# Kernel tuning notes

Hardware: AMD Instinct MI355X
Metric: run time of the kernel (lower is better)

## Reference

```python
import math
import jax, jax.numpy as jnp
import numpy as np

# ---------------- static structure (mirrors CG_woFilter_cuda + MyBatchNormWeightMM) ----------------
LMAX = 4
TAUS = [16, 16, 16, 16, 16]          # t_F: input channels per degree l
T_O  = [16, 16, 16, 16, 16]          # output channels per degree l after weight matmul
BN_EPS = 1e-5

# all (l, l1, l2) triples with l2 <= l1 <= lmax and |l1-l2| <= l <= min(l1+l2, lmax), sorted by (l,l1,l2)
TRIPLES = sorted([(l, l1, l2)
                  for l1 in range(LMAX + 1)
                  for l2 in range(l1 + 1)
                  for l in range(l1 - l2, min(l1 + l2, LMAX) + 1)])

T_FF = [0] * (LMAX + 1)              # t_FF[l] = sum over triples of taus[l1]*taus[l2]
for (l, l1, l2) in TRIPLES:
    T_FF[l] += TAUS[l1] * TAUS[l2]

def _cg_coef(j1, m1, j2, m2, j, m):
    """Clebsch-Gordan coefficient <j1 m1 j2 m2 | j m> (Condon-Shortley)."""
    if m1 + m2 != m:
        return 0.0
    f = math.factorial
    if j < abs(j1 - j2) or j > j1 + j2:
        return 0.0
    pref = math.sqrt((2 * j + 1) * f(j + j1 - j2) * f(j - j1 + j2) * f(j1 + j2 - j) / f(j1 + j2 + j + 1))
    pref *= math.sqrt(f(j + m) * f(j - m) * f(j1 - m1) * f(j1 + m1) * f(j2 - m2) * f(j2 + m2))
    s = 0.0
    for k in range(0, j1 + j2 - j + 1):
        if (j1 - m1 - k) < 0 or (j2 + m2 - k) < 0 or (j - j2 + m1 + k) < 0 or (j - j1 - m2 + k) < 0:
            continue
        s += ((-1.0) ** k) / (f(k) * f(j1 + j2 - j - k) * f(j1 - m1 - k)
                              * f(j2 + m2 - k) * f(j - j2 + m1 + k) * f(j - j1 - m2 + k))
    return pref * s

def _cg_matrix(l, l1, l2):
    C = np.zeros((2 * l + 1, 2 * l1 + 1, 2 * l2 + 1), dtype=np.float32)
    for m in range(-l, l + 1):
        for m1 in range(-l1, l1 + 1):
            m2 = m - m1
            if -l2 <= m2 <= l2:
                C[m + l, m1 + l1, m2 + l2] = _cg_coef(l1, m1, l2, m2, l, m)
    return C

CG_MATS = {t: jnp.asarray(_cg_matrix(*t)) for t in TRIPLES}

M_IN = sum(TAUS[l] * (2 * l + 1) for l in range(LMAX + 1))      # 400
W_LEN = sum(T_FF[l] * T_O[l] for l in range(LMAX + 1))          # 172032


def setup_inputs() -> dict:
    key = jax.random.key(0)
    k1, k2 = jax.random.split(key)
    B = 256
    Fs = jax.random.normal(k1, (B, M_IN, 2), dtype=jnp.float32)
    W = jax.random.normal(k2, (W_LEN, 2), dtype=jnp.float32) * 0.05
    return {"Fs": Fs, "W": W}


def reference(Fs, W):
    B = Fs.shape[0]
    # split input into per-degree blocks: F_l [B, tau, 2l+1, 2]
    Fl, off = [], 0
    for l in range(LMAX + 1):
        n = TAUS[l] * (2 * l + 1)
        Fl.append(Fs[:, off:off + n, :].reshape(B, TAUS[l], 2 * l + 1, 2))
        off += n
    # sparse CG tensor product: per-triple complex outer product contracted with CG coefs
    frags = [[] for _ in range(LMAX + 1)]
    for (l, l1, l2) in TRIPLES:
        C = CG_MATS[(l, l1, l2)]                     # [2l+1, 2l1+1, 2l2+1]
        a, b = Fl[l1], Fl[l2]
        ar, ai = a[..., 0], a[..., 1]
        br, bi = b[..., 0], b[..., 1]
        rr = jnp.einsum('bip,bjq,mpq->bijm', ar, br, C)
        ii = jnp.einsum('bip,bjq,mpq->bijm', ai, bi, C)
        ri = jnp.einsum('bip,bjq,mpq->bijm', ar, bi, C)
        ir = jnp.einsum('bip,bjq,mpq->bijm', ai, br, C)
        fr = (rr - ii).reshape(B, -1, 2 * l + 1)     # channels flattened as c1*tau2 + c2 (t_offsets order)
        fi = (ri + ir).reshape(B, -1, 2 * l + 1)
        frags[l].append(jnp.stack([fr, fi], axis=-1))
    # per-degree fragment batchnorm + complex weight matmul (FN_WMM)
    outs, woff = [], 0
    for l in range(LMAX + 1):
        FF = jnp.concatenate(frags[l], axis=1)       # [B, t_FF, 2l+1, 2]
        var = jnp.mean(jnp.sum(FF * FF, axis=-1), axis=(0, 2))      # per-channel mean |z|^2
        FFn = FF / (jnp.sqrt(var)[None, :, None, None] + BN_EPS)
        n = T_FF[l] * T_O[l]
        Wl = W[woff:woff + n].reshape(T_O[l], T_FF[l], 2)
        woff += n
        wr, wi = Wl[..., 0], Wl[..., 1]
        xr, xi = FFn[..., 0], FFn[..., 1]
        yr = jnp.einsum('oc,bcm->bom', wr, xr) - jnp.einsum('oc,bcm->bom', wi, xi)
        yi = jnp.einsum('oc,bcm->bom', wr, xi) + jnp.einsum('oc,bcm->bom', wi, xr)
        outs.append(jnp.stack([yr, yi], axis=-1).reshape(B, T_O[l] * (2 * l + 1), 2))
    return jnp.concatenate(outs, axis=1)             # [B, sum t_O[l]*(2l+1), 2] = [B, 400, 2]
```

## Files before the change

kernel.cpp:

```cpp
#include <hip/hip_runtime.h>
#include <math.h>

#define NTRI 42
#define NCH  10752
#define B_SZ 256

typedef float    f32x4 __attribute__((ext_vector_type(4)));
typedef _Float16 half8 __attribute__((ext_vector_type(8)));
typedef _Float16 f16x2 __attribute__((ext_vector_type(2)));

constexpr int CT_L [NTRI]={0,0,0,0,0, 1,1,1,1,1,1,1,1, 2,2,2,2,2,2,2,2,2,2, 3,3,3,3,3,3,3,3,3,3, 4,4,4,4,4,4,4,4,4};
constexpr int CT_L1[NTRI]={0,1,2,3,4, 1,1,2,2,3,3,4,4, 1,2,2,2,3,3,3,4,4,4, 2,2,3,3,3,3,4,4,4,4, 2,3,3,3,4,4,4,4,4};
constexpr int CT_L2[NTRI]={0,1,2,3,4, 0,1,1,2,2,3,3,4, 1,0,1,2,1,2,3,2,3,4, 1,2,0,1,2,3,1,2,3,4, 2,1,2,3,0,1,2,3,4};
constexpr int CT_T [NTRI]={0,1,2,3,4, 0,1,2,3,4,5,6,7, 0,1,2,3,4,5,6,7,8,9, 0,1,2,3,4,5,6,7,8,9, 0,1,2,3,4,5,6,7,8};

constexpr int KL_t[5]    ={1280,2048,2560,2560,2304};
constexpr int GBASE_t[5] ={0,1280,3328,5888,8448};
constexpr int ROFF_t[5]  ={0,16,64,144,256};
constexpr int NM_t[5]    ={1,3,5,7,9};
constexpr int FFB_t[5]   ={0,327680,1900544,5177344,9764864};
#define FF_TOT 15073280
constexpr int PL_t[5]    ={0,5,29,79,149};
#define PART_PL 4096
#define PART_TOT (230*PART_PL)

__device__ const int   dCTL[NTRI]={0,0,0,0,0, 1,1,1,1,1,1,1,1, 2,2,2,2,2,2,2,2,2,2, 3,3,3,3,3,3,3,3,3,3, 4,4,4,4,4,4,4,4,4};
__device__ const int   dCTT[NTRI]={0,1,2,3,4, 0,1,2,3,4,5,6,7, 0,1,2,3,4,5,6,7,8,9, 0,1,2,3,4,5,6,7,8,9, 0,1,2,3,4,5,6,7,8};
__device__ const int   dK[5]   ={1280,2048,2560,2560,2304};
__device__ const int   dWOFF[5]={0,20480,53248,94208,135168};
__device__ const int   dNM[5]  ={1,3,5,7,9};
__device__ const int   dFFB[5] ={0,327680,1900544,5177344,9764864};
__device__ const int   dPL[5]  ={0,5,29,79,149};
__device__ const int   dGB[5]  ={0,1280,3328,5888,8448};
__device__ const int   dROFF[5]={0,16,64,144,256};
__device__ const int   dNT[5]  ={5,8,10,10,9};
__device__ const float dINV[5] ={1.f/256.f,1.f/768.f,1.f/1280.f,1.f/1792.f,1.f/2304.f};

__device__ float  g_varsum[NCH];
__device__ __align__(16) f16x2  g_ff[FF_TOT];
__device__ float2 g_part[PART_TOT];

constexpr double cfact(int n){ double r=1.0; for(int i=2;i<=n;i++) r*=(double)i; return r; }
constexpr double csqrt_(double v){ double x = v>1.0? v:1.0; for(int i=0;i<80;i++) x = 0.5*(x+v/x); return x; }
constexpr double ccg(int j1,int m1,int j2,int m2,int j,int m){
    if(m1+m2!=m) return 0.0;
    double pref = csqrt_((2.0*j+1.0)*cfact(j+j1-j2)*cfact(j-j1+j2)*cfact(j1+j2-j)/cfact(j1+j2+j+1));
    pref *= csqrt_(cfact(j+m)*cfact(j-m)*cfact(j1-m1)*cfact(j1+m1)*cfact(j2-m2)*cfact(j2+m2));
    double s=0.0;
    for(int k=0;k<=j1+j2-j;k++){
        int a=j1-m1-k, bb=j2+m2-k, c=j-j2+m1+k, d=j-j1-m2+k;
        if(a<0||bb<0||c<0||d<0) continue;
        double term = 1.0/(cfact(k)*cfact(j1+j2-j-k)*cfact(a)*cfact(bb)*cfact(c)*cfact(d));
        s += (k&1)? -term : term;
    }
    return pref*s;
}
struct CG81 { float a[81]; };
constexpr CG81 makecg(int l,int l1,int l2){
    CG81 t{};
    const int n1=2*l1+1;
    for(int mi=0;mi<2*l+1;mi++)
        for(int p=0;p<n1;p++){
            const int m=mi-l, m1=p-l1, m2=m-m1;
            if(m2>=-l2 && m2<=l2) t.a[mi*n1+p]=(float)ccg(l1,m1,l2,m2,l,m);
        }
    return t;
}
template<int TR> struct CGC { static constexpr CG81 t = makecg(CT_L[TR],CT_L1[TR],CT_L2[TR]); };

template<int TR>
__device__ __forceinline__ void cg_compute(const float2* __restrict__ FsB,
                                           int i, int j, float2* __restrict__ ff){
    constexpr int L=CT_L[TR], L1=CT_L1[TR], L2=CT_L2[TR];
    constexpr int N1=2*L1+1, N2=2*L2+1, NM=2*L+1;
    float2 A[N1], Bv[N2];
    #pragma unroll
    for(int p=0;p<N1;p++) A[p]=FsB[ROFF_t[L1]+i*N1+p];
    #pragma unroll
    for(int q=0;q<N2;q++) Bv[q]=FsB[ROFF_t[L2]+j*N2+q];
    #pragma unroll
    for(int mi=0;mi<NM;mi++){
        float aR=0.f, aI=0.f;
        const int pLo = (mi-L+L1-L2) > 0 ? (mi-L+L1-L2) : 0;
        const int pHi = (mi-L+L1+L2) < 2*L1 ? (mi-L+L1+L2) : 2*L1;
        #pragma unroll
        for(int p=0;p<N1;p++){
            if(p>=pLo && p<=pHi){
                const float c = CGC<TR>::t.a[mi*N1+p];
                if(c != 0.f){
                    const int q = mi - L - p + L1 + L2;
                    const float2 a=A[p], b=Bv[q];
                    aR = fmaf(c, a.x*b.x - a.y*b.y, aR);
                    aI = fmaf(c, a.x*b.y + a.y*b.x, aI);
                }
            }
        }
        ff[mi]=make_float2(aR,aI);
    }
}

template<int TR>
__device__ __forceinline__ void cg_one(const float2* __restrict__ Fs, int bc, int t){
    constexpr int L=CT_L[TR], NM=2*L+1, T=CT_T[TR], K=KL_t[L];
    constexpr int MPL=256*K;
    const int i=t>>4, j=t&15;
    float n2=0.f;
    for(int b4=0;b4<4;b4++){
        const int b=bc*4+b4;
        float2 ff[NM];
        cg_compute<TR>(Fs + b*400, i, j, ff);
        const int base = FFB_t[L] + b*K + T*256 + t;
        #pragma unroll
        for(int m=0;m<NM;m++){
            n2 = fmaf(ff[m].x,ff[m].x,n2);
            n2 = fmaf(ff[m].y,ff[m].y,n2);
            f16x2 h; h.x=(_Float16)ff[m].x; h.y=(_Float16)ff[m].y;
            g_ff[base + m*MPL] = h;
        }
    }
    atomicAdd(&g_varsum[GBASE_t[L] + CT_T[TR]*256 + t], n2);
}

template<int TR>
__device__ __forceinline__ void cg_disp(int tr, const float2* Fs, int bc, int t){
    if constexpr (TR < NTRI){
        if(tr==TR) cg_one<TR>(Fs,bc,t);
        else       cg_disp<TR+1>(tr,Fs,bc,t);
    }
}

__global__ void __launch_bounds__(256) k_cg(const float2* __restrict__ Fs){
    cg_disp<0>(blockIdx.x, Fs, blockIdx.y, threadIdx.x);
}

__global__ void __launch_bounds__(64) k_mm(const float2* __restrict__ W2){
    const int tr=blockIdx.x, bg=blockIdx.y, m=blockIdx.z;
    const int l=dCTL[tr];
    const int NM=dNM[l];
    if(m>=NM) return;
    const int T=dCTT[tr], K=dK[l];
    const int lane=threadIdx.x;
    const int l15=lane&15, kg=lane>>4;
    const float4* __restrict__ Wv = reinterpret_cast<const float4*>(W2 + dWOFF[l] + l15*K) + T*128 + kg*2;
    const float4* __restrict__ Vv = reinterpret_cast<const float4*>(g_varsum + dGB[l] + T*256) + kg;
    const f16x2*  __restrict__ Xp = g_ff + dFFB[l] + m*(256*K) + (bg*16 + l15)*K + T*256 + kg*4;
    const float inv = dINV[l];
    f32x4 ar0={0.f,0.f,0.f,0.f}, ar1={0.f,0.f,0.f,0.f};
    f32x4 ai0={0.f,0.f,0.f,0.f}, ai1={0.f,0.f,0.f,0.f};
    #pragma unroll
    for(int ks=0; ks<16; ks++){
        const float4 wa = Wv[ks*8];
        const float4 wb = Wv[ks*8+1];
        const float4 vs = Vv[ks*4];
        const float s0 = 1.f/(sqrtf(vs.x*inv)+1e-5f);
        const float s1 = 1.f/(sqrtf(vs.y*inv)+1e-5f);
        const float s2 = 1.f/(sqrtf(vs.z*inv)+1e-5f);
        const float s3 = 1.f/(sqrtf(vs.w*inv)+1e-5f);
        half8 Ar, Ai;
        Ar[0]=(_Float16)( wa.x*s0); Ar[1]=(_Float16)(-wa.y*s0);
        Ar[2]=(_Float16)( wa.z*s1); Ar[3]=(_Float16)(-wa.w*s1);
        Ar[4]=(_Float16)( wb.x*s2); Ar[5]=(_Float16)(-wb.y*s2);
        Ar[6]=(_Float16)( wb.z*s3); Ar[7]=(_Float16)(-wb.w*s3);
        Ai[0]=(_Float16)( wa.y*s0); Ai[1]=(_Float16)( wa.x*s0);
        Ai[2]=(_Float16)( wa.w*s1); Ai[3]=(_Float16)( wa.z*s1);
        Ai[4]=(_Float16)( wb.y*s2); Ai[5]=(_Float16)( wb.x*s2);
        Ai[6]=(_Float16)( wb.w*s3); Ai[7]=(_Float16)( wb.z*s3);
        const half8 Bf = *reinterpret_cast<const half8*>(Xp + ks*16);
        if(ks & 1){
            ar1 = __builtin_amdgcn_mfma_f32_16x16x32_f16(Ar, Bf, ar1, 0,0,0);
            ai1 = __builtin_amdgcn_mfma_f32_16x16x32_f16(Ai, Bf, ai1, 0,0,0);
        } else {
            ar0 = __builtin_amdgcn_mfma_f32_16x16x32_f16(Ar, Bf, ar0, 0,0,0);
            ai0 = __builtin_amdgcn_mfma_f32_16x16x32_f16(Ai, Bf, ai0, 0,0,0);
        }
    }
    const f32x4 ar = ar0 + ar1, ai = ai0 + ai1;
    float2* __restrict__ pp = g_part + (dPL[l] + T*NM + m)*PART_PL + bg*256;
    #pragma unroll
    for(int r=0;r<4;r++){
        pp[(kg*4+r)*16 + l15] = make_float2(ar[r], ai[r]);
    }
}

__global__ void __launch_bounds__(448) k_red(float2* __restrict__ out){
    const int b=blockIdx.x, r=threadIdx.x;
    if(r>=400) return;
    const int l = (r<16)?0:(r<64)?1:(r<144)?2:(r<256)?3:4;
    const int om = r - dROFF[l];
    const int nm = dNM[l];
    const int o = om/nm, m = om - o*nm;
    const float2* __restrict__ pp = g_part + (dPL[l]+m)*PART_PL + (b>>4)*256 + o*16 + (b&15);
    float2 s=make_float2(0.f,0.f);
    const int nt=dNT[l];
    for(int T=0;T<nt;T++){
        const float2 v = pp[T*nm*PART_PL];
        s.x+=v.x; s.y+=v.y;
    }
    out[b*400+r]=s;
}

extern "C" void kernel_launch(void* const* d_in, const int* in_sizes, int n_in,
                              void* d_out, int out_size, void* d_ws, size_t ws_size,
                              hipStream_t stream){
    const float2* Fs = (const float2*)d_in[0];
    const float2* W  = (const float2*)d_in[1];
    float2* out = (float2*)d_out;

    void* dvs=nullptr;
    hipGetSymbolAddress(&dvs, HIP_SYMBOL(g_varsum));
    hipMemsetAsync(dvs, 0, NCH*sizeof(float), stream);

    k_cg <<<dim3(NTRI,64),   256, 0, stream>>>(Fs);
    k_mm <<<dim3(NTRI,16,9),  64, 0, stream>>>(W);
    k_red<<<dim3(B_SZ),      448, 0, stream>>>(out);
}
```

Measured before the change: 121.3 us.

## Precompute normalized fp16 weights in separate kernel, drop atomics and memset

```diff
diff --git a/kernel.cpp b/kernel.cpp
--- a/kernel.cpp
+++ b/kernel.cpp
@@ -4,6 +4,7 @@
 #define NTRI 42
 #define NCH  10752
 #define B_SZ 256
+#define AH_PL 172032
 
 typedef float    f32x4 __attribute__((ext_vector_type(4)));
 typedef _Float16 half8 __attribute__((ext_vector_type(8)));
@@ -17,7 +18,6 @@
 constexpr int KL_t[5]    ={1280,2048,2560,2560,2304};
 constexpr int GBASE_t[5] ={0,1280,3328,5888,8448};
 constexpr int ROFF_t[5]  ={0,16,64,144,256};
-constexpr int NM_t[5]    ={1,3,5,7,9};
 constexpr int FFB_t[5]   ={0,327680,1900544,5177344,9764864};
 #define FF_TOT 15073280
 constexpr int PL_t[5]    ={0,5,29,79,149};
@@ -36,8 +36,9 @@
 __device__ const int   dNT[5]  ={5,8,10,10,9};
 __device__ const float dINV[5] ={1.f/256.f,1.f/768.f,1.f/1280.f,1.f/1792.f,1.f/2304.f};
 
-__device__ float  g_varsum[NCH];
+__device__ float  g_vpart[64*NCH];
 __device__ __align__(16) f16x2  g_ff[FF_TOT];
+__device__ __align__(16) f16x2  g_ah[2*AH_PL];
 __device__ float2 g_part[PART_TOT];
 
 constexpr double cfact(int n){ double r=1.0; for(int i=2;i<=n;i++) r*=(double)i; return r; }
@@ -118,7 +119,7 @@
             g_ff[base + m*MPL] = h;
         }
     }
-    atomicAdd(&g_varsum[GBASE_t[L] + CT_T[TR]*256 + t], n2);
+    g_vpart[bc*NCH + GBASE_t[L] + CT_T[TR]*256 + t] = n2;
 }
 
 template<int TR>
@@ -133,39 +134,46 @@
     cg_disp<0>(blockIdx.x, Fs, blockIdx.y, threadIdx.x);
 }
 
-__global__ void __launch_bounds__(64) k_mm(const float2* __restrict__ W2){
-    const int tr=blockIdx.x, bg=blockIdx.y, m=blockIdx.z;
-    const int l=dCTL[tr];
-    const int NM=dNM[l];
-    if(m>=NM) return;
-    const int T=dCTT[tr], K=dK[l];
-    const int lane=threadIdx.x;
+__global__ void __launch_bounds__(256) k_wn(const float2* __restrict__ W2){
+    const int tr=blockIdx.x, t=threadIdx.x;
+    const int l=dCTL[tr], T=dCTT[tr], K=dK[l];
+    const int ch = dGB[l] + T*256 + t;
+    float s=0.f;
+    #pragma unroll 8
+    for(int bc=0;bc<64;bc++) s += g_vpart[bc*NCH + ch];
+    const float invv = 1.f/(sqrtf(s*dINV[l])+1e-5f);
+    const int base = dWOFF[l] + T*256 + t;
+    #pragma unroll 4
+    for(int o=0;o<16;o++){
+        const float2 w = W2[base + o*K];
+        f16x2 hr, hi;
+        hr.x=(_Float16)( w.x*invv); hr.y=(_Float16)(-w.y*invv);
+        hi.x=(_Float16)( w.y*invv); hi.y=(_Float16)( w.x*invv);
+        g_ah[base + o*K]         = hr;
+        g_ah[AH_PL + base + o*K] = hi;
+    }
+}
+
+__global__ void __launch_bounds__(256) k_mm(){
+    const int j=blockIdx.x;
+    const int wv=threadIdx.x>>6, lane=threadIdx.x&63;
+    const int bg=blockIdx.y*4+wv;
+    const int l=(j<5)?0:(j<29)?1:(j<79)?2:(j<149)?3:4;
+    const int nm=dNM[l];
+    const int loc=j-dPL[l];
+    const int T=loc/nm, m=loc-T*nm;
+    const int K=dK[l];
     const int l15=lane&15, kg=lane>>4;
-    const float4* __restrict__ Wv = reinterpret_cast<const float4*>(W2 + dWOFF[l] + l15*K) + T*128 + kg*2;
-    const float4* __restrict__ Vv = reinterpret_cast<const float4*>(g_varsum + dGB[l] + T*256) + kg;
-    const f16x2*  __restrict__ Xp = g_ff + dFFB[l] + m*(256*K) + (bg*16 + l15)*K + T*256 + kg*4;
-    const float inv = dINV[l];
+    const half8* __restrict__ Arp = reinterpret_cast<const half8*>(g_ah + dWOFF[l] + l15*K + T*256 + kg*4);
+    const half8* __restrict__ Aip = reinterpret_cast<const half8*>(g_ah + AH_PL + dWOFF[l] + l15*K + T*256 + kg*4);
+    const half8* __restrict__ Xp  = reinterpret_cast<const half8*>(g_ff + dFFB[l] + m*(K<<8) + (bg*16+l15)*K + T*256 + kg*4);
     f32x4 ar0={0.f,0.f,0.f,0.f}, ar1={0.f,0.f,0.f,0.f};
     f32x4 ai0={0.f,0.f,0.f,0.f}, ai1={0.f,0.f,0.f,0.f};
     #pragma unroll
     for(int ks=0; ks<16; ks++){
-        const float4 wa = Wv[ks*8];
-        const float4 wb = Wv[ks*8+1];
-        const float4 vs = Vv[ks*4];
-        const float s0 = 1.f/(sqrtf(vs.x*inv)+1e-5f);
-        const float s1 = 1.f/(sqrtf(vs.y*inv)+1e-5f);
-        const float s2 = 1.f/(sqrtf(vs.z*inv)+1e-5f);
-        const float s3 = 1.f/(sqrtf(vs.w*inv)+1e-5f);
-        half8 Ar, Ai;
-        Ar[0]=(_Float16)( wa.x*s0); Ar[1]=(_Float16)(-wa.y*s0);
-        Ar[2]=(_Float16)( wa.z*s1); Ar[3]=(_Float16)(-wa.w*s1);
-        Ar[4]=(_Float16)( wb.x*s2); Ar[5]=(_Float16)(-wb.y*s2);
-        Ar[6]=(_Float16)( wb.z*s3); Ar[7]=(_Float16)(-wb.w*s3);
-        Ai[0]=(_Float16)( wa.y*s0); Ai[1]=(_Float16)( wa.x*s0);
-        Ai[2]=(_Float16)( wa.w*s1); Ai[3]=(_Float16)( wa.z*s1);
-        Ai[4]=(_Float16)( wb.y*s2); Ai[5]=(_Float16)( wb.x*s2);
-        Ai[6]=(_Float16)( wb.w*s3); Ai[7]=(_Float16)( wb.z*s3);
-        const half8 Bf = *reinterpret_cast<const half8*>(Xp + ks*16);
+        const half8 Ar = Arp[ks*4];
+        const half8 Ai = Aip[ks*4];
+        const half8 Bf = Xp [ks*4];
         if(ks & 1){
             ar1 = __builtin_amdgcn_mfma_f32_16x16x32_f16(Ar, Bf, ar1, 0,0,0);
             ai1 = __builtin_amdgcn_mfma_f32_16x16x32_f16(Ai, Bf, ai1, 0,0,0);
@@ -175,7 +183,7 @@
         }
     }
     const f32x4 ar = ar0 + ar1, ai = ai0 + ai1;
-    float2* __restrict__ pp = g_part + (dPL[l] + T*NM + m)*PART_PL + bg*256;
+    float2* __restrict__ pp = g_part + j*PART_PL + bg*256;
     #pragma unroll
     for(int r=0;r<4;r++){
         pp[(kg*4+r)*16 + l15] = make_float2(ar[r], ai[r]);
@@ -206,11 +214,8 @@
     const float2* W  = (const float2*)d_in[1];
     float2* out = (float2*)d_out;
 
-    void* dvs=nullptr;
-    hipGetSymbolAddress(&dvs, HIP_SYMBOL(g_varsum));
-    hipMemsetAsync(dvs, 0, NCH*sizeof(float), stream);
-
-    k_cg <<<dim3(NTRI,64),   256, 0, stream>>>(Fs);
-    k_mm <<<dim3(NTRI,16,9),  64, 0, stream>>>(W);
-    k_red<<<dim3(B_SZ),      448, 0, stream>>>(out);
-}
+    k_cg <<<dim3(NTRI,64), 256, 0, stream>>>(Fs);
+    k_wn <<<dim3(NTRI),    256, 0, stream>>>(W);
+    k_mm <<<dim3(230,4),   256, 0, stream>>>();
+    k_red<<<dim3(B_SZ),    448, 0, stream>>>(out);
+}
```

Measured after the change: 121.3 us. Within noise of the previous version (+0.0%).
